# Optimization experiments

Hardware: AMD Instinct MI355X
Metric: run time of the kernel (lower is better)

The kernel has to match this reference:

```python
import jax, jax.numpy as jnp
import numpy as np
from jax import lax

B, T = 64, 2048
D_ENC, D_RNN, D_ATT = 512, 1024, 128
NF, K = 32, 31


def setup_inputs() -> dict:
    key = jax.random.key(0)
    ks = jax.random.split(key, 9)
    return {
        "attention_hidden_state": jax.random.normal(ks[0], (B, D_RNN), jnp.float32),
        "memory": jax.random.normal(ks[1], (B, T, D_ENC), jnp.float32),
        "processed_memory": jax.random.normal(ks[2], (B, T, D_ATT), jnp.float32),
        "attention_weights_cat": jax.random.uniform(ks[3], (B, 2, T), jnp.float32),
        "mask": jnp.zeros((B, T), dtype=bool),
        "query_w": jax.random.normal(ks[4], (D_ATT, D_RNN), jnp.float32) * 0.02,
        "value_w": jax.random.normal(ks[5], (1, D_ATT), jnp.float32) * 0.05,
        "loc_conv_w": jax.random.normal(ks[6], (NF, 2, K), jnp.float32) * 0.1,
        "loc_dense_w": jax.random.normal(ks[7], (D_ATT, NF), jnp.float32) * 0.1,
    }


def reference(attention_hidden_state, memory, processed_memory,
              attention_weights_cat, mask, query_w, value_w,
              loc_conv_w, loc_dense_w):
    k = loc_conv_w.shape[-1]
    pad = (k - 1) // 2
    # processed query: [B, 1, D_ATT]
    pq = (attention_hidden_state @ query_w.T)[:, None, :]
    # location features: Conv1d(2->NF, 'same' pad, no bias) then dense NF->D_ATT
    loc = lax.conv_general_dilated(
        attention_weights_cat, loc_conv_w,
        window_strides=(1,), padding=[(pad, pad)],
        dimension_numbers=("NCH", "OIH", "NCH"))  # [B, NF, T]
    loc = jnp.einsum("bft,af->bta", loc, loc_dense_w)  # [B, T, D_ATT]
    # additive energies
    energies = jnp.tanh(pq + processed_memory + loc)  # [B, T, D_ATT]
    alignment = jnp.einsum("bta,a->bt", energies, value_w[0])  # [B, T]
    alignment = jnp.where(mask, -jnp.inf, alignment)
    attention_weights = jax.nn.softmax(alignment, axis=1)  # [B, T]
    attention_context = jnp.einsum("bt,btd->bd", attention_weights, memory)
    return attention_context, attention_weights
```

## Files before the change

kernel.cpp:

```cpp
#include <hip/hip_runtime.h>
#include <hip/hip_bf16.h>

#define BB 64
#define TT 2048
#define D_ENC 512
#define D_RNN 1024
#define D_ATT 128
#define NF 32
#define KW 31

__device__ __forceinline__ float fast_tanh(float x) {
    float e = __expf(2.0f * x);
    return 1.0f - __fdividef(2.0f, e + 1.0f);
}

__global__ __launch_bounds__(256) void pq_kernel(
    const float* __restrict__ hid, const float* __restrict__ qw,
    float* __restrict__ pq)
{
    int b = blockIdx.x;
    int wave = threadIdx.x >> 6, lane = threadIdx.x & 63;
    int a = blockIdx.y * 4 + wave;
    const float* hrow = hid + (size_t)b * D_RNN;
    const float* qrow = qw + (size_t)a * D_RNN;
    float acc = 0.f;
#pragma unroll
    for (int j = 0; j < 4; ++j) {
        int k = (j * 64 + lane) * 4;
        float4 h = *(const float4*)(hrow + k);
        float4 q = *(const float4*)(qrow + k);
        acc += h.x * q.x + h.y * q.y + h.z * q.z + h.w * q.w;
    }
#pragma unroll
    for (int off = 32; off; off >>= 1) acc += __shfl_xor(acc, off, 64);
    if (lane == 0) pq[b * D_ATT + a] = acc;
}

__global__ __launch_bounds__(256) void align_kernel(
    const float* __restrict__ pm,
    const float* __restrict__ awcat,
    const unsigned char* __restrict__ mask,
    const float* __restrict__ convw,
    const float* __restrict__ ldw,
    const float* __restrict__ vw,
    const float* __restrict__ pq,
    float* __restrict__ align_out)
{
    __shared__ float s_aw[2 * 160];
    __shared__ float s_loc[128 * NF];

    int b = blockIdx.x;
    int t0 = blockIdx.y * 128;
    int tid = threadIdx.x;

    for (int i = tid; i < 320; i += 256) {
        int c = i / 160, j = i % 160;
        int tg = t0 - 15 + j;
        float v = 0.f;
        if (tg >= 0 && tg < TT) v = awcat[((size_t)b * 2 + c) * TT + tg];
        s_aw[c * 160 + j] = v;
    }
    __syncthreads();

    {
        int f = tid & 31, g = tid >> 5;
        float w[2 * KW];
#pragma unroll
        for (int j = 0; j < 2 * KW; ++j) w[j] = convw[f * 2 * KW + j];
#pragma unroll
        for (int p = 0; p < 4; ++p) {
            int tb = g * 16 + p * 4;
            float a0 = 0.f, a1 = 0.f, a2 = 0.f, a3 = 0.f;
#pragma unroll
            for (int c = 0; c < 2; ++c) {
                float x[34];
#pragma unroll
                for (int j = 0; j < 34; ++j) x[j] = s_aw[c * 160 + tb + j];
#pragma unroll
                for (int k = 0; k < KW; ++k) {
                    float wk = w[c * KW + k];
                    a0 += x[k] * wk; a1 += x[k + 1] * wk;
                    a2 += x[k + 2] * wk; a3 += x[k + 3] * wk;
                }
            }
            s_loc[(tb + 0) * NF + f] = a0;
            s_loc[(tb + 1) * NF + f] = a1;
            s_loc[(tb + 2) * NF + f] = a2;
            s_loc[(tb + 3) * NF + f] = a3;
        }
    }
    __syncthreads();

    int wave = tid >> 6, lane = tid & 63;
    float pq0 = pq[b * 128 + lane], pq1 = pq[b * 128 + 64 + lane];
    float vw0 = vw[lane], vw1 = vw[64 + lane];
    float4 lA[8], lB[8];
#pragma unroll
    for (int f4 = 0; f4 < 8; ++f4) {
        lA[f4] = *(const float4*)(ldw + lane * NF + f4 * 4);
        lB[f4] = *(const float4*)(ldw + (64 + lane) * NF + f4 * 4);
    }
    const float* pmb = pm + ((size_t)b * TT + t0) * 128;
    for (int i = 0; i < 32; ++i) {
        int t = wave * 32 + i;
        float pm0 = pmb[(size_t)t * 128 + lane];
        float pm1 = pmb[(size_t)t * 128 + 64 + lane];
        float dA = 0.f, dB = 0.f;
#pragma unroll
        for (int f4 = 0; f4 < 8; ++f4) {
            float4 lv = *(const float4*)&s_loc[t * NF + f4 * 4];
            dA += lv.x * lA[f4].x + lv.y * lA[f4].y + lv.z * lA[f4].z + lv.w * lA[f4].w;
            dB += lv.x * lB[f4].x + lv.y * lB[f4].y + lv.z * lB[f4].z + lv.w * lB[f4].w;
        }
        float eA = fast_tanh(pq0 + pm0 + dA);
        float eB = fast_tanh(pq1 + pm1 + dB);
        float al = vw0 * eA + vw1 * eB;
#pragma unroll
        for (int off = 32; off; off >>= 1) al += __shfl_xor(al, off, 64);
        if (lane == 0) {
            int tt = t0 + t;
            bool m = mask[(size_t)b * TT + tt] != 0;
            align_out[(size_t)b * TT + tt] = m ? -__builtin_inff() : al;
        }
    }
}

__global__ __launch_bounds__(256) void softmax_kernel(float* __restrict__ wts)
{
    int b = blockIdx.x;
    int tid = threadIdx.x;
    float* row = wts + (size_t)b * TT;
    float v[8];
    float mx = -__builtin_inff();
#pragma unroll
    for (int i = 0; i < 8; ++i) { v[i] = row[tid + i * 256]; mx = fmaxf(mx, v[i]); }
    __shared__ float s_red[8];
    int wave = tid >> 6, lane = tid & 63;
#pragma unroll
    for (int off = 32; off; off >>= 1) mx = fmaxf(mx, __shfl_xor(mx, off, 64));
    if (lane == 0) s_red[wave] = mx;
    __syncthreads();
    mx = fmaxf(fmaxf(s_red[0], s_red[1]), fmaxf(s_red[2], s_red[3]));
    float sum = 0.f;
#pragma unroll
    for (int i = 0; i < 8; ++i) { v[i] = __expf(v[i] - mx); sum += v[i]; }
#pragma unroll
    for (int off = 32; off; off >>= 1) sum += __shfl_xor(sum, off, 64);
    if (lane == 0) s_red[4 + wave] = sum;
    __syncthreads();
    sum = s_red[4] + s_red[5] + s_red[6] + s_red[7];
    float inv = __fdividef(1.0f, sum);
#pragma unroll
    for (int i = 0; i < 8; ++i) row[tid + i * 256] = v[i] * inv;
}

__global__ __launch_bounds__(256) void ctx_kernel(
    const float* __restrict__ mem, const float* __restrict__ wts,
    float* __restrict__ out)
{
    int b = blockIdx.x, c = blockIdx.y;
    int tid = threadIdx.x;
    int d4 = tid & 127;
    int th = tid >> 7;
    int t0 = c * 128;
    const float* wrow = wts + (size_t)b * TT + t0;
    const float4* mrow = (const float4*)(mem + ((size_t)b * TT + t0) * D_ENC);
    float4 acc = {0.f, 0.f, 0.f, 0.f};
    for (int i = th; i < 128; i += 2) {
        float w = wrow[i];
        float4 m = mrow[(size_t)i * 128 + d4];
        acc.x += w * m.x; acc.y += w * m.y; acc.z += w * m.z; acc.w += w * m.w;
    }
    __shared__ float4 s_p[128];
    if (th == 1) s_p[d4] = acc;
    __syncthreads();
    if (th == 0) {
        float4 o = s_p[d4];
        float* dst = out + (size_t)b * D_ENC + d4 * 4;
        atomicAdd(dst + 0, acc.x + o.x);
        atomicAdd(dst + 1, acc.y + o.y);
        atomicAdd(dst + 2, acc.z + o.z);
        atomicAdd(dst + 3, acc.w + o.w);
    }
}

extern "C" void kernel_launch(void* const* d_in, const int* in_sizes, int n_in,
                              void* d_out, int out_size, void* d_ws, size_t ws_size,
                              hipStream_t stream)
{
    const float* hid  = (const float*)d_in[0];
    const float* mem  = (const float*)d_in[1];
    const float* pm   = (const float*)d_in[2];
    const float* aw   = (const float*)d_in[3];
    const unsigned char* mask = (const unsigned char*)d_in[4];
    const float* qw   = (const float*)d_in[5];
    const float* vw   = (const float*)d_in[6];
    const float* cw   = (const float*)d_in[7];
    const float* ldw  = (const float*)d_in[8];

    float* out = (float*)d_out;
    float* ctx = out;
    float* wts = out + BB * D_ENC;
    float* pq  = (float*)d_ws;

    hipMemsetAsync(ctx, 0, (size_t)BB * D_ENC * sizeof(float), stream);
    pq_kernel<<<dim3(BB, 32), 256, 0, stream>>>(hid, qw, pq);
    align_kernel<<<dim3(BB, TT / 128), 256, 0, stream>>>(pm, aw, mask, cw, ldw, vw, pq, wts);
    softmax_kernel<<<BB, 256, 0, stream>>>(wts);
    ctx_kernel<<<dim3(BB, 16), 256, 0, stream>>>(mem, wts, ctx);
}
```

Measured before the change: 492.6 us.

## Fuse alignment, local softmax and context into split-softmax kernel with combine pass

Merges the alignment, softmax and context kernels into one per-chunk kernel. Each chunk computes its local max and sum and an unnormalized partial context, and a small combine kernel rescales the partials into the final context and weights, flash-decoding style. This removes the global round-trip of alignments, two kernel launches, the memset and the atomics. In exchange it adds workspace traffic for the partial contexts and the unnormalized weights, and a chunk whose positions are all masked yields a zero contribution.

```diff
diff --git a/kernel.cpp b/kernel.cpp
--- a/kernel.cpp
+++ b/kernel.cpp
@@ -1,5 +1,4 @@
 #include <hip/hip_runtime.h>
-#include <hip/hip_bf16.h>
 
 #define BB 64
 #define TT 2048
@@ -8,6 +7,8 @@
 #define D_ATT 128
 #define NF 32
 #define KW 31
+#define NCHUNK 16
+#define TCHUNK 128
 
 __device__ __forceinline__ float fast_tanh(float x) {
     float e = __expf(2.0f * x);
@@ -36,7 +37,7 @@
     if (lane == 0) pq[b * D_ATT + a] = acc;
 }
 
-__global__ __launch_bounds__(256) void align_kernel(
+__global__ __launch_bounds__(256) void fused_kernel(
     const float* __restrict__ pm,
     const float* __restrict__ awcat,
     const unsigned char* __restrict__ mask,
@@ -44,21 +45,31 @@
     const float* __restrict__ ldw,
     const float* __restrict__ vw,
     const float* __restrict__ pq,
-    float* __restrict__ align_out)
+    const float* __restrict__ mem,
+    float* __restrict__ pmat,
+    float* __restrict__ pc,
+    float* __restrict__ sm,
+    float* __restrict__ ss)
 {
     __shared__ float s_aw[2 * 160];
-    __shared__ float s_loc[128 * NF];
+    __shared__ float s_loc[TCHUNK * NF];
+    __shared__ float s_al[TCHUNK];
+    __shared__ float s_p[TCHUNK];
+    __shared__ float s_red[8];
+    __shared__ float4 s_pc[128];
 
     int b = blockIdx.x;
-    int t0 = blockIdx.y * 128;
+    int c = blockIdx.y;
+    int t0 = c * TCHUNK;
     int tid = threadIdx.x;
+    int wave = tid >> 6, lane = tid & 63;
 
     for (int i = tid; i < 320; i += 256) {
-        int c = i / 160, j = i % 160;
+        int ch = i / 160, j = i % 160;
         int tg = t0 - 15 + j;
         float v = 0.f;
-        if (tg >= 0 && tg < TT) v = awcat[((size_t)b * 2 + c) * TT + tg];
-        s_aw[c * 160 + j] = v;
+        if (tg >= 0 && tg < TT) v = awcat[((size_t)b * 2 + ch) * TT + tg];
+        s_aw[ch * 160 + j] = v;
     }
     __syncthreads();
 
@@ -68,17 +79,17 @@
 #pragma unroll
         for (int j = 0; j < 2 * KW; ++j) w[j] = convw[f * 2 * KW + j];
 #pragma unroll
-        for (int p = 0; p < 4; ++p) {
-            int tb = g * 16 + p * 4;
+        for (int p4 = 0; p4 < 4; ++p4) {
+            int tb = g * 16 + p4 * 4;
             float a0 = 0.f, a1 = 0.f, a2 = 0.f, a3 = 0.f;
 #pragma unroll
-            for (int c = 0; c < 2; ++c) {
+            for (int ch = 0; ch < 2; ++ch) {
                 float x[34];
 #pragma unroll
-                for (int j = 0; j < 34; ++j) x[j] = s_aw[c * 160 + tb + j];
+                for (int j = 0; j < 34; ++j) x[j] = s_aw[ch * 160 + tb + j];
 #pragma unroll
                 for (int k = 0; k < KW; ++k) {
-                    float wk = w[c * KW + k];
+                    float wk = w[ch * KW + k];
                     a0 += x[k] * wk; a1 += x[k + 1] * wk;
                     a2 += x[k + 2] * wk; a3 += x[k + 3] * wk;
                 }
@@ -91,96 +102,113 @@
     }
     __syncthreads();
 
-    int wave = tid >> 6, lane = tid & 63;
-    float pq0 = pq[b * 128 + lane], pq1 = pq[b * 128 + 64 + lane];
-    float vw0 = vw[lane], vw1 = vw[64 + lane];
-    float4 lA[8], lB[8];
-#pragma unroll
-    for (int f4 = 0; f4 < 8; ++f4) {
-        lA[f4] = *(const float4*)(ldw + lane * NF + f4 * 4);
-        lB[f4] = *(const float4*)(ldw + (64 + lane) * NF + f4 * 4);
-    }
-    const float* pmb = pm + ((size_t)b * TT + t0) * 128;
-    for (int i = 0; i < 32; ++i) {
-        int t = wave * 32 + i;
-        float pm0 = pmb[(size_t)t * 128 + lane];
-        float pm1 = pmb[(size_t)t * 128 + 64 + lane];
-        float dA = 0.f, dB = 0.f;
+    {
+        float pq0 = pq[b * 128 + lane], pq1 = pq[b * 128 + 64 + lane];
+        float vw0 = vw[lane], vw1 = vw[64 + lane];
+        float4 lA[8], lB[8];
 #pragma unroll
         for (int f4 = 0; f4 < 8; ++f4) {
-            float4 lv = *(const float4*)&s_loc[t * NF + f4 * 4];
-            dA += lv.x * lA[f4].x + lv.y * lA[f4].y + lv.z * lA[f4].z + lv.w * lA[f4].w;
-            dB += lv.x * lB[f4].x + lv.y * lB[f4].y + lv.z * lB[f4].z + lv.w * lB[f4].w;
-        }
-        float eA = fast_tanh(pq0 + pm0 + dA);
-        float eB = fast_tanh(pq1 + pm1 + dB);
-        float al = vw0 * eA + vw1 * eB;
-#pragma unroll
-        for (int off = 32; off; off >>= 1) al += __shfl_xor(al, off, 64);
-        if (lane == 0) {
-            int tt = t0 + t;
-            bool m = mask[(size_t)b * TT + tt] != 0;
-            align_out[(size_t)b * TT + tt] = m ? -__builtin_inff() : al;
-        }
-    }
-}
-
-__global__ __launch_bounds__(256) void softmax_kernel(float* __restrict__ wts)
-{
-    int b = blockIdx.x;
-    int tid = threadIdx.x;
-    float* row = wts + (size_t)b * TT;
-    float v[8];
-    float mx = -__builtin_inff();
-#pragma unroll
-    for (int i = 0; i < 8; ++i) { v[i] = row[tid + i * 256]; mx = fmaxf(mx, v[i]); }
-    __shared__ float s_red[8];
-    int wave = tid >> 6, lane = tid & 63;
+            lA[f4] = *(const float4*)(ldw + lane * NF + f4 * 4);
+            lB[f4] = *(const float4*)(ldw + (64 + lane) * NF + f4 * 4);
+        }
+        const float* pmb = pm + ((size_t)b * TT + t0) * 128;
+        for (int i = 0; i < 32; ++i) {
+            int t = wave * 32 + i;
+            float pm0 = pmb[(size_t)t * 128 + lane];
+            float pm1 = pmb[(size_t)t * 128 + 64 + lane];
+            float dA = 0.f, dB = 0.f;
+#pragma unroll
+            for (int f4 = 0; f4 < 8; ++f4) {
+                float4 lv = *(const float4*)&s_loc[t * NF + f4 * 4];
+                dA += lv.x * lA[f4].x + lv.y * lA[f4].y + lv.z * lA[f4].z + lv.w * lA[f4].w;
+                dB += lv.x * lB[f4].x + lv.y * lB[f4].y + lv.z * lB[f4].z + lv.w * lB[f4].w;
+            }
+            float eA = fast_tanh(pq0 + pm0 + dA);
+            float eB = fast_tanh(pq1 + pm1 + dB);
+            float al = vw0 * eA + vw1 * eB;
+#pragma unroll
+            for (int off = 32; off; off >>= 1) al += __shfl_xor(al, off, 64);
+            if (lane == 0) {
+                bool mk = mask[(size_t)b * TT + t0 + t] != 0;
+                s_al[t] = mk ? -__builtin_inff() : al;
+            }
+        }
+    }
+    __syncthreads();
+
+    float val = (tid < TCHUNK) ? s_al[tid] : -__builtin_inff();
+    float mx = val;
 #pragma unroll
     for (int off = 32; off; off >>= 1) mx = fmaxf(mx, __shfl_xor(mx, off, 64));
     if (lane == 0) s_red[wave] = mx;
     __syncthreads();
-    mx = fmaxf(fmaxf(s_red[0], s_red[1]), fmaxf(s_red[2], s_red[3]));
-    float sum = 0.f;
-#pragma unroll
-    for (int i = 0; i < 8; ++i) { v[i] = __expf(v[i] - mx); sum += v[i]; }
+    float M = fmaxf(fmaxf(s_red[0], s_red[1]), fmaxf(s_red[2], s_red[3]));
+    float p = (tid < TCHUNK && M > -__builtin_inff()) ? __expf(val - M) : 0.f;
+    float sum = p;
 #pragma unroll
     for (int off = 32; off; off >>= 1) sum += __shfl_xor(sum, off, 64);
     if (lane == 0) s_red[4 + wave] = sum;
-    __syncthreads();
-    sum = s_red[4] + s_red[5] + s_red[6] + s_red[7];
-    float inv = __fdividef(1.0f, sum);
-#pragma unroll
-    for (int i = 0; i < 8; ++i) row[tid + i * 256] = v[i] * inv;
-}
-
-__global__ __launch_bounds__(256) void ctx_kernel(
-    const float* __restrict__ mem, const float* __restrict__ wts,
-    float* __restrict__ out)
-{
-    int b = blockIdx.x, c = blockIdx.y;
-    int tid = threadIdx.x;
-    int d4 = tid & 127;
-    int th = tid >> 7;
-    int t0 = c * 128;
-    const float* wrow = wts + (size_t)b * TT + t0;
-    const float4* mrow = (const float4*)(mem + ((size_t)b * TT + t0) * D_ENC);
-    float4 acc = {0.f, 0.f, 0.f, 0.f};
-    for (int i = th; i < 128; i += 2) {
-        float w = wrow[i];
-        float4 m = mrow[(size_t)i * 128 + d4];
-        acc.x += w * m.x; acc.y += w * m.y; acc.z += w * m.z; acc.w += w * m.w;
-    }
-    __shared__ float4 s_p[128];
-    if (th == 1) s_p[d4] = acc;
-    __syncthreads();
-    if (th == 0) {
-        float4 o = s_p[d4];
-        float* dst = out + (size_t)b * D_ENC + d4 * 4;
-        atomicAdd(dst + 0, acc.x + o.x);
-        atomicAdd(dst + 1, acc.y + o.y);
-        atomicAdd(dst + 2, acc.z + o.z);
-        atomicAdd(dst + 3, acc.w + o.w);
+    if (tid < TCHUNK) s_p[tid] = p;
+    __syncthreads();
+    if (tid < TCHUNK) pmat[(size_t)b * TT + t0 + tid] = p;
+    if (tid == 0) {
+        sm[b * NCHUNK + c] = M;
+        ss[b * NCHUNK + c] = s_red[4] + s_red[5] + s_red[6] + s_red[7];
+    }
+
+    {
+        int d4 = tid & 127, th = tid >> 7;
+        const float4* mrow = (const float4*)(mem + ((size_t)b * TT + t0) * D_ENC);
+        float4 acc = {0.f, 0.f, 0.f, 0.f};
+        for (int i = th; i < TCHUNK; i += 2) {
+            float w = s_p[i];
+            float4 m4 = mrow[(size_t)i * 128 + d4];
+            acc.x += w * m4.x; acc.y += w * m4.y;
+            acc.z += w * m4.z; acc.w += w * m4.w;
+        }
+        if (th == 1) s_pc[d4] = acc;
+        __syncthreads();
+        if (th == 0) {
+            float4 o = s_pc[d4];
+            float4 r = {acc.x + o.x, acc.y + o.y, acc.z + o.z, acc.w + o.w};
+            ((float4*)(pc + ((size_t)b * NCHUNK + c) * D_ENC))[d4] = r;
+        }
+    }
+}
+
+__global__ __launch_bounds__(256) void combine_kernel(
+    const float* __restrict__ pmat, const float* __restrict__ pc,
+    const float* __restrict__ sm, const float* __restrict__ ss,
+    float* __restrict__ ctx, float* __restrict__ wts)
+{
+    int b = blockIdx.x, tid = threadIdx.x;
+    __shared__ float s_f[NCHUNK];
+    if (tid < 64) {
+        float m = (tid < NCHUNK) ? sm[b * NCHUNK + tid] : -__builtin_inff();
+        float M = m;
+#pragma unroll
+        for (int off = 32; off; off >>= 1) M = fmaxf(M, __shfl_xor(M, off, 64));
+        float e = (tid < NCHUNK) ? __expf(m - M) : 0.f;
+        float z = (tid < NCHUNK) ? ss[b * NCHUNK + tid] * e : 0.f;
+        float Z = z;
+#pragma unroll
+        for (int off = 32; off; off >>= 1) Z += __shfl_xor(Z, off, 64);
+        if (tid < NCHUNK) s_f[tid] = e * __fdividef(1.f, Z);
+    }
+    __syncthreads();
+    float2 acc = {0.f, 0.f};
+    const float2* pcb = (const float2*)(pc + (size_t)b * NCHUNK * D_ENC);
+#pragma unroll
+    for (int c2 = 0; c2 < NCHUNK; ++c2) {
+        float2 v = pcb[(size_t)c2 * 256 + tid];
+        float f = s_f[c2];
+        acc.x += v.x * f; acc.y += v.y * f;
+    }
+    ((float2*)(ctx + (size_t)b * D_ENC))[tid] = acc;
+#pragma unroll
+    for (int i = 0; i < 8; ++i) {
+        int t = tid + i * 256;
+        wts[(size_t)b * TT + t] = pmat[(size_t)b * TT + t] * s_f[t >> 7];
     }
 }
 
@@ -201,11 +229,16 @@
     float* out = (float*)d_out;
     float* ctx = out;
     float* wts = out + BB * D_ENC;
-    float* pq  = (float*)d_ws;
-
-    hipMemsetAsync(ctx, 0, (size_t)BB * D_ENC * sizeof(float), stream);
+
+    float* ws   = (float*)d_ws;
+    float* pq   = ws;
+    float* pmat = pq + BB * D_ATT;
+    float* pc   = pmat + (size_t)BB * TT;
+    float* sm   = pc + (size_t)BB * NCHUNK * D_ENC;
+    float* ss   = sm + BB * NCHUNK;
+
     pq_kernel<<<dim3(BB, 32), 256, 0, stream>>>(hid, qw, pq);
-    align_kernel<<<dim3(BB, TT / 128), 256, 0, stream>>>(pm, aw, mask, cw, ldw, vw, pq, wts);
-    softmax_kernel<<<BB, 256, 0, stream>>>(wts);
-    ctx_kernel<<<dim3(BB, 16), 256, 0, stream>>>(mem, wts, ctx);
-}
+    fused_kernel<<<dim3(BB, NCHUNK), 256, 0, stream>>>(
+        pm, aw, mask, cw, ldw, vw, pq, mem, pmat, pc, sm, ss);
+    combine_kernel<<<BB, 256, 0, stream>>>(pmat, pc, sm, ss, ctx, wts);
+}
```

Result: no change. 501.8 us (+1.9%).
